# Kernel optimization log

Measured on AMD Instinct MI355X. Metric: run time of the kernel, lower is better.

Reference implementation:

```python
import jax, jax.numpy as jnp
import numpy as np

B, S, D, H = 4, 1024, 1024, 16
HD = D // H


def setup_inputs() -> dict:
    key = jax.random.key(0)
    ks = jax.random.split(key, 8)
    x = jax.random.normal(ks[0], (B, S, D), dtype=jnp.float32)
    attn_bias = jax.random.normal(ks[1], (B, H, S, S), dtype=jnp.float32) * 0.1
    pos_ids = jnp.broadcast_to(jnp.arange(S, dtype=jnp.int32), (B, S))
    lengths = jnp.array([S, S - 64, S - 128, S - 256], dtype=jnp.int32)
    pad_mask = jnp.arange(S)[None, :] >= lengths[:, None]  # True = padded key
    scale = 0.02
    Wq = jax.random.normal(ks[2], (D, D), dtype=jnp.float32) * scale
    Wk = jax.random.normal(ks[3], (D, D), dtype=jnp.float32) * scale
    Wv = jax.random.normal(ks[4], (D, D), dtype=jnp.float32) * scale
    Wo = jax.random.normal(ks[5], (D, D), dtype=jnp.float32) * scale
    bq = jnp.zeros((D,), jnp.float32); bk = jnp.zeros((D,), jnp.float32)
    bv = jnp.zeros((D,), jnp.float32); bo = jnp.zeros((D,), jnp.float32)
    return {"x": x, "attn_bias": attn_bias, "pos_ids": pos_ids, "pad_mask": pad_mask,
            "Wq": Wq, "bq": bq, "Wk": Wk, "bk": bk, "Wv": Wv, "bv": bv, "Wo": Wo, "bo": bo}


def _apply_rotary(q, k, pos_ids):
    # q,k: [B,S,H,HD]; pos_ids: [B,S]
    hd = q.shape[-1]
    inv_freq = 1.0 / (10000.0 ** (jnp.arange(0, hd, 2, dtype=jnp.float32) / hd))
    freqs = pos_ids.astype(jnp.float32)[:, :, None] * inv_freq  # [B,S,HD/2]
    emb = jnp.concatenate([freqs, freqs], axis=-1)[:, :, None, :]  # [B,S,1,HD]
    cos, sin = jnp.cos(emb), jnp.sin(emb)
    def rot_half(t):
        t1, t2 = jnp.split(t, 2, axis=-1)
        return jnp.concatenate([-t2, t1], axis=-1)
    return q * cos + rot_half(q) * sin, k * cos + rot_half(k) * sin


def reference(x, attn_bias, pos_ids, pad_mask, Wq, bq, Wk, bk, Wv, bv, Wo, bo):
    b, s, d = x.shape
    q = (x @ Wq.T + bq).reshape(b, s, H, HD)
    k = (x @ Wk.T + bk).reshape(b, s, H, HD)
    v = (x @ Wv.T + bv).reshape(b, s, H, HD)
    q, k = _apply_rotary(q, k, pos_ids)
    q = q.transpose(0, 2, 1, 3)  # [B,H,S,HD]
    k = k.transpose(0, 2, 1, 3)
    v = v.transpose(0, 2, 1, 3)
    scores = jnp.einsum("bhqd,bhkd->bhqk", q, k) / np.sqrt(HD).astype(np.float32)
    scores = scores + attn_bias
    scores = jnp.where(pad_mask[:, None, None, :], -jnp.inf, scores)
    attn = jax.nn.softmax(scores, axis=-1)  # dropout p=0 -> identity
    out = jnp.einsum("bhqk,bhkd->bqhd", attn, v).reshape(b, s, d)
    metric = k.mean(axis=1)  # mean over heads -> [B,S,HD]
    return out @ Wo.T + bo, metric
```

## Files before the change

kernel.cpp:

```cpp
#include <hip/hip_runtime.h>
#include <hip/hip_bf16.h>

#define SS 1024
#define DD 1024
#define HH 16
#define HDD 64

using f32x4  = __attribute__((ext_vector_type(4))) float;
using bf16x8 = __attribute__((ext_vector_type(8))) __bf16;
using bf16x4 = __attribute__((ext_vector_type(4))) __bf16;

__device__ __forceinline__ void gload_lds16(const void* g, void* l) {
  __builtin_amdgcn_global_load_lds((__attribute__((address_space(1))) void*)g,
                                   (__attribute__((address_space(3))) void*)l, 16, 0, 0);
}

__global__ void convert_kernel(const float4* __restrict__ x, const float4* __restrict__ Wq,
                               const float4* __restrict__ Wk, const float4* __restrict__ Wv,
                               const float4* __restrict__ Wo,
                               bf16x4* __restrict__ xb, bf16x4* __restrict__ wqkvb,
                               bf16x4* __restrict__ wob, float4* __restrict__ metric) {
  int i = blockIdx.x * 256 + threadIdx.x;
  if (blockIdx.x < 256) {
    float4 z = {0.f, 0.f, 0.f, 0.f};
    metric[blockIdx.x * 256 + threadIdx.x] = z;
  }
  float4 v; bf16x4* dst;
  if (i < 1048576)      { v = x[i];              dst = xb + i; }
  else if (i < 1310720) { v = Wq[i - 1048576];   dst = wqkvb + (i - 1048576); }
  else if (i < 1572864) { v = Wk[i - 1310720];   dst = wqkvb + 262144 + (i - 1310720); }
  else if (i < 1835008) { v = Wv[i - 1572864];   dst = wqkvb + 524288 + (i - 1572864); }
  else                  { v = Wo[i - 1835008];   dst = wob + (i - 1835008); }
  bf16x4 o;
  o[0] = (__bf16)v.x; o[1] = (__bf16)v.y; o[2] = (__bf16)v.z; o[3] = (__bf16)v.w;
  *dst = o;
}

template<int EPI, int TN>
__global__ __launch_bounds__(256, 3)
void gemm_kernel(const __bf16* __restrict__ A, const __bf16* __restrict__ Bm, int N,
                 const float* __restrict__ b0, const float* __restrict__ b1,
                 const float* __restrict__ b2, const int* __restrict__ pos_ids,
                 __bf16* __restrict__ Qr, __bf16* __restrict__ Kr, __bf16* __restrict__ Vtg,
                 float* __restrict__ metric, float* __restrict__ Cout) {
  __shared__ __align__(16) char smem[17408];
  __bf16* As = (__bf16*)smem;
  __bf16* Bs = (__bf16*)(smem + 8192);
  constexpr int NJ = TN / 32;
  const int tid = threadIdx.x;
  const int wid = tid >> 6, lane = tid & 63;
  const int g = lane >> 4, cl = lane & 15;
  const int ntn = N / TN;
  const int tile = (blockIdx.x & 7) * ((int)gridDim.x >> 3) + (blockIdx.x >> 3);
  const int bm = tile / ntn, bn = tile % ntn;
  const int m0 = bm << 7, n0 = bn * TN;
  const int wr = (wid >> 1) << 6, wc = (wid & 1) * (TN / 2);

  f32x4 acc[4][NJ] = {};

  for (int kk = 0; kk < 1024; kk += 32) {
    __syncthreads();
#pragma unroll
    for (int p = 0; p < 2; ++p) {
      int idx = p * 256 + tid;
      gload_lds16(A + (size_t)(m0 + (idx >> 2)) * 1024 + kk + ((idx & 3) << 3),
                  (char*)As + p * 4096 + wid * 1024);
    }
#pragma unroll
    for (int p = 0; p < TN / 64; ++p) {
      int idx = p * 256 + tid;
      gload_lds16(Bm + (size_t)(n0 + (idx >> 2)) * 1024 + kk + ((idx & 3) << 3),
                  (char*)Bs + p * 4096 + wid * 1024);
    }
    __syncthreads();
    bf16x8 fa[4], fb[NJ];
#pragma unroll
    for (int i = 0; i < 4; ++i)
      fa[i] = *(const bf16x8*)(As + (wr + i * 16 + cl) * 32 + g * 8);
#pragma unroll
    for (int j = 0; j < NJ; ++j)
      fb[j] = *(const bf16x8*)(Bs + (wc + j * 16 + cl) * 32 + g * 8);
#pragma unroll
    for (int i = 0; i < 4; ++i)
#pragma unroll
      for (int j = 0; j < NJ; ++j)
        acc[i][j] = __builtin_amdgcn_mfma_f32_16x16x32_bf16(fa[i], fb[j], acc[i][j], 0, 0, 0);
  }

  if constexpr (EPI == 1) {
#pragma unroll
    for (int j = 0; j < NJ; ++j) {
      int col = n0 + wc + j * 16 + cl;
      float bv = b0[col];
#pragma unroll
      for (int i = 0; i < 4; ++i)
#pragma unroll
        for (int r = 0; r < 4; ++r) {
          int row = m0 + wr + i * 16 + g * 4 + r;
          Cout[(size_t)row * 1024 + col] = acc[i][j][r] + bv;
        }
    }
  } else if (n0 >= 2048) {
    __bf16* vt_s = (__bf16*)smem;
    const int b_ = m0 >> 10, s0 = m0 & 1023;
    const int vbase = n0 - 2048;
#pragma unroll
    for (int phase = 0; phase < 2; ++phase) {
      __syncthreads();
      if ((wid & 1) == phase) {
#pragma unroll
        for (int j = 0; j < 4; ++j) {
          int d = j * 16 + cl;
          float bv = b2[vbase + wc + d];
#pragma unroll
          for (int i = 0; i < 4; ++i)
#pragma unroll
            for (int r = 0; r < 4; ++r)
              vt_s[d * 136 + wr + i * 16 + g * 4 + r] = (__bf16)(acc[i][j][r] + bv);
        }
      }
      __syncthreads();
      int hh = (vbase >> 6) + phase;
#pragma unroll
      for (int p = 0; p < 4; ++p) {
        int d = p * 16 + (tid >> 4), s8 = (tid & 15) * 8;
        bf16x8 v = *(const bf16x8*)(vt_s + d * 136 + s8);
        *(bf16x8*)(Vtg + ((size_t)(b_ * HH + hh) * HDD + d) * SS + s0 + s8) = v;
      }
    }
  } else {
    const int cb = n0 + wc;
    const int region = cb >> 10;
    const int hcol = (cb & 1023) >> 6;
    const int cir = cb & 1023;
    const float* bias = region == 0 ? b0 : b1;
    __bf16* dst = region == 0 ? Qr : Kr;
    float invf0 = exp2f(-0.4152410118609203f * (float)(cl));
    float invf1 = exp2f(-0.4152410118609203f * (float)(16 + cl));
#pragma unroll
    for (int i = 0; i < 4; ++i) {
#pragma unroll
      for (int r = 0; r < 4; ++r) {
        int row = m0 + wr + i * 16 + g * 4 + r;
        int b_ = row >> 10, s = row & 1023;
        size_t ob = ((size_t)(b_ * HH + hcol) * SS + s) * HDD;
        float pos = (float)pos_ids[row];
#pragma unroll
        for (int j = 0; j < 2; ++j) {
          int dlo = j * 16 + cl;
          float vlo = acc[i][j][r]     + bias[cir + dlo];
          float vhi = acc[i][j + 2][r] + bias[cir + dlo + 32];
          float th = pos * (j == 0 ? invf0 : invf1);
          float sn, cs;
          __sincosf(th, &sn, &cs);
          float olo = vlo * cs - vhi * sn;
          float ohi = vhi * cs + vlo * sn;
          dst[ob + dlo]      = (__bf16)olo;
          dst[ob + dlo + 32] = (__bf16)ohi;
          if (region == 1) {
            atomicAdd(&metric[(size_t)row * HDD + dlo],      olo * 0.0625f);
            atomicAdd(&metric[(size_t)row * HDD + dlo + 32], ohi * 0.0625f);
          }
        }
      }
    }
  }
}

#define TILE_BODY(T, BUF, BCUR, BNXT)                                              \
  {                                                                                \
    __syncthreads();                                                               \
    if ((T) + 1 < ntile) {                                                         \
      const int kk = ((T) + 1) * 64;                                               \
      gload_lds16(Kb + (size_t)(kk + krow) * 64 + kchk * 8,                        \
                  (char*)&Ks[(BUF) ^ 1][8 * wid][0]);                              \
      gload_lds16(Vb + (size_t)krow * SS + kk + kchk * 8,                          \
                  (char*)&Vt[(BUF) ^ 1][8 * wid][0]);                              \
      _Pragma("unroll") for (int kt = 0; kt < 4; ++kt)                             \
        _Pragma("unroll") for (int r = 0; r < 4; ++r)                              \
          BNXT[kt][r] = Bb[(size_t)(q0 + 4 * g + r) * SS + kk + kt * 16 + cl];     \
    }                                                                              \
    f32x4 sc[4];                                                                   \
    __builtin_amdgcn_s_setprio(1);                                                 \
    _Pragma("unroll") for (int kt = 0; kt < 4; ++kt) {                             \
      bf16x8 kb0 = *(const bf16x8*)(&Ks[(BUF)][kt * 16 + cl][(g ^ swz) * 8]);      \
      bf16x8 kb1 = *(const bf16x8*)(&Ks[(BUF)][kt * 16 + cl][((g + 4) ^ swz) * 8]);\
      f32x4 z = {0.f, 0.f, 0.f, 0.f};                                              \
      z = __builtin_amdgcn_mfma_f32_16x16x32_bf16(aq0, kb0, z, 0, 0, 0);           \
      sc[kt] = __builtin_amdgcn_mfma_f32_16x16x32_bf16(aq1, kb1, z, 0, 0, 0);      \
    }                                                                              \
    __builtin_amdgcn_s_setprio(0);                                                 \
    _Pragma("unroll") for (int kt = 0; kt < 4; ++kt)                               \
      _Pragma("unroll") for (int r = 0; r < 4; ++r)                                \
        sc[kt][r] = sc[kt][r] * 0.125f + BCUR[kt][r];                              \
    float mx[4];                                                                   \
    _Pragma("unroll") for (int r = 0; r < 4; ++r)                                  \
      mx[r] = fmaxf(fmaxf(sc[0][r], sc[1][r]), fmaxf(sc[2][r], sc[3][r]));         \
    _Pragma("unroll") for (int d = 1; d < 16; d <<= 1)                             \
      _Pragma("unroll") for (int r = 0; r < 4; ++r)                                \
        mx[r] = fmaxf(mx[r], __shfl_xor(mx[r], d, 64));                            \
    bool adv = true;                                                               \
    _Pragma("unroll") for (int r = 0; r < 4; ++r)                                  \
      adv = adv && (mx[r] <= m_l[r] + 8.0f);                                       \
    if (!__all(adv)) {                                                             \
      _Pragma("unroll") for (int r = 0; r < 4; ++r) {                              \
        float nm = fmaxf(m_l[r], mx[r]);                                           \
        float s_ = __expf(m_l[r] - nm);                                            \
        m_l[r] = nm; l_l[r] *= s_;                                                 \
        _Pragma("unroll") for (int dj = 0; dj < 4; ++dj) o[dj][r] *= s_;           \
      }                                                                            \
    }                                                                              \
    _Pragma("unroll") for (int kt = 0; kt < 4; ++kt)                               \
      _Pragma("unroll") for (int r = 0; r < 4; ++r)                                \
        sc[kt][r] = __expf(sc[kt][r] - m_l[r]);                                    \
    _Pragma("unroll") for (int kt = 0; kt < 4; ++kt)                               \
      _Pragma("unroll") for (int r = 0; r < 4; ++r)                                \
        Plds[wid][g * 4 + r][kt * 16 + cl] = (__bf16)sc[kt][r];                    \
    bf16x8 pa0 = *(const bf16x8*)(&Plds[wid][cl][g * 8]);                          \
    bf16x8 pa1 = *(const bf16x8*)(&Plds[wid][cl][32 + g * 8]);                     \
    __builtin_amdgcn_s_setprio(1);                                                 \
    f32x4 ls = {0.f, 0.f, 0.f, 0.f};                                               \
    ls = __builtin_amdgcn_mfma_f32_16x16x32_bf16(pa0, onesb, ls, 0, 0, 0);         \
    ls = __builtin_amdgcn_mfma_f32_16x16x32_bf16(pa1, onesb, ls, 0, 0, 0);         \
    _Pragma("unroll") for (int dj = 0; dj < 4; ++dj) {                             \
      bf16x8 vb0 = *(const bf16x8*)(&Vt[(BUF)][dj * 16 + cl][(g ^ swz) * 8]);      \
      bf16x8 vb1 = *(const bf16x8*)(&Vt[(BUF)][dj * 16 + cl][((g + 4) ^ swz) * 8]);\
      o[dj] = __builtin_amdgcn_mfma_f32_16x16x32_bf16(pa0, vb0, o[dj], 0, 0, 0);   \
      o[dj] = __builtin_amdgcn_mfma_f32_16x16x32_bf16(pa1, vb1, o[dj], 0, 0, 0);   \
    }                                                                              \
    __builtin_amdgcn_s_setprio(0);                                                 \
    _Pragma("unroll") for (int r = 0; r < 4; ++r) l_l[r] += ls[r];                 \
  }

__global__ __launch_bounds__(512, 4)
void attn_kernel(const __bf16* __restrict__ Qr, const __bf16* __restrict__ Kr,
                 const __bf16* __restrict__ Vtg, const float* __restrict__ bias,
                 const int* __restrict__ pad, __bf16* __restrict__ attn_out) {
  __shared__ __align__(16) __bf16 Ks[2][64][64];
  __shared__ __align__(16) __bf16 Vt[2][64][64];
  __shared__ __align__(16) __bf16 Plds[8][16][68];
  const int tid = threadIdx.x;
  const int wid = tid >> 6, lane = tid & 63;
  const int g = lane >> 4, cl = lane & 15;
  const int bh = blockIdx.x & 63, b_ = bh >> 4, h = bh & 15;
  const int q0 = (blockIdx.x >> 6) * 128 + wid * 16;
  const __bf16* Qb = Qr  + ((size_t)bh << 16);
  const __bf16* Kb = Kr  + ((size_t)bh << 16);
  const __bf16* Vb = Vtg + ((size_t)bh << 16);
  const float*  Bb = bias + ((size_t)bh << 20);
  const int* padb = pad + b_ * SS;

  int pm = (lane < 16) ? padb[lane * 64] : 1;
  unsigned long long ball = __ballot(pm == 0);
  const int ntile = __popcll(ball & 0xFFFFull);

  const int l8 = lane >> 3, l7 = lane & 7;
  const int krow = 8 * wid + l8;
  const int kchk = l7 ^ l8;
  const int swz = cl & 7;

  gload_lds16(Kb + (size_t)krow * 64 + kchk * 8, (char*)&Ks[0][8 * wid][0]);
  gload_lds16(Vb + (size_t)krow * SS + kchk * 8, (char*)&Vt[0][8 * wid][0]);
  float bregA[4][4], bregB[4][4];
#pragma unroll
  for (int kt = 0; kt < 4; ++kt)
#pragma unroll
    for (int r = 0; r < 4; ++r)
      bregA[kt][r] = Bb[(size_t)(q0 + 4 * g + r) * SS + kt * 16 + cl];

  bf16x8 aq0 = *(const bf16x8*)(Qb + (size_t)(q0 + cl) * 64 + g * 8);
  bf16x8 aq1 = *(const bf16x8*)(Qb + (size_t)(q0 + cl) * 64 + 32 + g * 8);
  bf16x8 onesb;
#pragma unroll
  for (int j = 0; j < 8; ++j) onesb[j] = (__bf16)1.0f;

  f32x4 o[4] = {};
  float m_l[4] = {-1e30f, -1e30f, -1e30f, -1e30f};
  float l_l[4] = {0.f, 0.f, 0.f, 0.f};

  for (int t = 0; t < ntile; t += 2) {
    TILE_BODY(t, 0, bregA, bregB);
    if (t + 1 < ntile) TILE_BODY(t + 1, 1, bregB, bregA);
  }

#pragma unroll
  for (int dj = 0; dj < 4; ++dj)
#pragma unroll
    for (int r = 0; r < 4; ++r) {
      int qrow = q0 + g * 4 + r;
      attn_out[(size_t)(b_ * SS + qrow) * DD + h * 64 + dj * 16 + cl] =
          (__bf16)(o[dj][r] / l_l[r]);
    }
}

extern "C" void kernel_launch(void* const* d_in, const int* in_sizes, int n_in,
                              void* d_out, int out_size, void* d_ws, size_t ws_size,
                              hipStream_t stream) {
  const float* x  = (const float*)d_in[0];
  const float* ab = (const float*)d_in[1];
  const int* pos  = (const int*)d_in[2];
  const int* pad  = (const int*)d_in[3];
  const float* Wq = (const float*)d_in[4];
  const float* bq = (const float*)d_in[5];
  const float* Wk = (const float*)d_in[6];
  const float* bk = (const float*)d_in[7];
  const float* Wv = (const float*)d_in[8];
  const float* bv = (const float*)d_in[9];
  const float* Wo = (const float*)d_in[10];
  const float* bo = (const float*)d_in[11];
  float* out = (float*)d_out;
  float* metric = out + 4194304;

  char* ws = (char*)d_ws;
  __bf16* Qr   = (__bf16*)(ws);
  __bf16* Kr   = (__bf16*)(ws + 8388608);
  __bf16* Vtg  = (__bf16*)(ws + 16777216);
  __bf16* xb   = (__bf16*)(ws + 25165824);
  __bf16* wqkv = (__bf16*)(ws + 33554432);
  __bf16* wob  = (__bf16*)(ws + 39845888);
  __bf16* ao   = (__bf16*)(ws + 41943040);

  convert_kernel<<<8192, 256, 0, stream>>>((const float4*)x, (const float4*)Wq,
                                           (const float4*)Wk, (const float4*)Wv,
                                           (const float4*)Wo, (bf16x4*)xb,
                                           (bf16x4*)wqkv, (bf16x4*)wob, (float4*)metric);
  gemm_kernel<0, 128><<<768, 256, 0, stream>>>(xb, wqkv, 3072, bq, bk, bv, pos,
                                               Qr, Kr, Vtg, metric, nullptr);
  attn_kernel<<<512, 512, 0, stream>>>(Qr, Kr, Vtg, ab, pad, ao);
  gemm_kernel<1, 64><<<512, 256, 0, stream>>>(ao, wob, 1024, bo, nullptr, nullptr, nullptr,
                                              nullptr, nullptr, nullptr, nullptr, out);
}
```

Baseline: 173.6 us.

## Double-buffer GEMM LDS tiles with K=64 stages and XOR swizzle

Restructures the bf16 GEMM main loop to use two 32KB LDS buffers with K-step 64, prefetching the next stage via global_load_lds while MFMAs consume the current one, and uses one barrier per iteration. Adds an XOR swizzle on the 16-byte chunk index to reduce LDS bank conflicts on fragment reads. The output projection switches from 128x64 to 128x128 tiles, halving its grid to 256 blocks. The 64KB LDS per block and launch bounds of 2 lower occupancy, and the smaller out-proj grid may underfill the CUs.

Measured after the change: 161.1 us. -7.2%, faster.

```diff
diff --git a/kernel.cpp b/kernel.cpp
--- a/kernel.cpp
+++ b/kernel.cpp
@@ -36,60 +36,69 @@
   *dst = o;
 }
 
-template<int EPI, int TN>
-__global__ __launch_bounds__(256, 3)
+#define GEMM_STAGE(BUF, KK)                                                        \
+  {                                                                                \
+    char* Ab = smem + (BUF) * 32768;                                               \
+    char* Bb = Ab + 16384;                                                         \
+    _Pragma("unroll") for (int q = 0; q < 4; ++q) {                                \
+      int idx = q * 256 + tid;                                                     \
+      int row = idx >> 3, c = idx & 7;                                             \
+      gload_lds16(A  + (size_t)(m0 + row) * 1024 + (KK) + ((c ^ (row & 7)) << 3),  \
+                  Ab + q * 4096 + wid * 1024);                                     \
+      gload_lds16(Bm + (size_t)(n0 + row) * 1024 + (KK) + ((c ^ (row & 7)) << 3),  \
+                  Bb + q * 4096 + wid * 1024);                                     \
+    }                                                                              \
+  }
+
+template<int EPI>
+__global__ __launch_bounds__(256, 2)
 void gemm_kernel(const __bf16* __restrict__ A, const __bf16* __restrict__ Bm, int N,
                  const float* __restrict__ b0, const float* __restrict__ b1,
                  const float* __restrict__ b2, const int* __restrict__ pos_ids,
                  __bf16* __restrict__ Qr, __bf16* __restrict__ Kr, __bf16* __restrict__ Vtg,
                  float* __restrict__ metric, float* __restrict__ Cout) {
-  __shared__ __align__(16) char smem[17408];
-  __bf16* As = (__bf16*)smem;
-  __bf16* Bs = (__bf16*)(smem + 8192);
-  constexpr int NJ = TN / 32;
+  __shared__ __align__(16) char smem[65536];
   const int tid = threadIdx.x;
   const int wid = tid >> 6, lane = tid & 63;
   const int g = lane >> 4, cl = lane & 15;
-  const int ntn = N / TN;
+  const int ntn = N >> 7;
   const int tile = (blockIdx.x & 7) * ((int)gridDim.x >> 3) + (blockIdx.x >> 3);
   const int bm = tile / ntn, bn = tile % ntn;
-  const int m0 = bm << 7, n0 = bn * TN;
-  const int wr = (wid >> 1) << 6, wc = (wid & 1) * (TN / 2);
-
-  f32x4 acc[4][NJ] = {};
-
-  for (int kk = 0; kk < 1024; kk += 32) {
+  const int m0 = bm << 7, n0 = bn << 7;
+  const int wr = (wid >> 1) << 6, wc = (wid & 1) << 6;
+  const int swz = cl & 7;
+
+  f32x4 acc[4][4] = {};
+
+  GEMM_STAGE(0, 0);
+  __syncthreads();
+  int buf = 0;
+  for (int t = 0; t < 16; ++t) {
+    if (t + 1 < 16) GEMM_STAGE(buf ^ 1, (t + 1) * 64);
+    const __bf16* Abuf = (const __bf16*)(smem + buf * 32768);
+    const __bf16* Bbuf = Abuf + 8192;
+#pragma unroll
+    for (int s = 0; s < 2; ++s) {
+      bf16x8 fa[4], fb[4];
+#pragma unroll
+      for (int i = 0; i < 4; ++i)
+        fa[i] = *(const bf16x8*)(Abuf + (wr + i * 16 + cl) * 64 + (((s * 4 + g) ^ swz) << 3));
+#pragma unroll
+      for (int j = 0; j < 4; ++j)
+        fb[j] = *(const bf16x8*)(Bbuf + (wc + j * 16 + cl) * 64 + (((s * 4 + g) ^ swz) << 3));
+#pragma unroll
+      for (int i = 0; i < 4; ++i)
+#pragma unroll
+        for (int j = 0; j < 4; ++j)
+          acc[i][j] = __builtin_amdgcn_mfma_f32_16x16x32_bf16(fa[i], fb[j], acc[i][j], 0, 0, 0);
+    }
     __syncthreads();
-#pragma unroll
-    for (int p = 0; p < 2; ++p) {
-      int idx = p * 256 + tid;
-      gload_lds16(A + (size_t)(m0 + (idx >> 2)) * 1024 + kk + ((idx & 3) << 3),
-                  (char*)As + p * 4096 + wid * 1024);
-    }
-#pragma unroll
-    for (int p = 0; p < TN / 64; ++p) {
-      int idx = p * 256 + tid;
-      gload_lds16(Bm + (size_t)(n0 + (idx >> 2)) * 1024 + kk + ((idx & 3) << 3),
-                  (char*)Bs + p * 4096 + wid * 1024);
-    }
-    __syncthreads();
-    bf16x8 fa[4], fb[NJ];
-#pragma unroll
-    for (int i = 0; i < 4; ++i)
-      fa[i] = *(const bf16x8*)(As + (wr + i * 16 + cl) * 32 + g * 8);
-#pragma unroll
-    for (int j = 0; j < NJ; ++j)
-      fb[j] = *(const bf16x8*)(Bs + (wc + j * 16 + cl) * 32 + g * 8);
-#pragma unroll
-    for (int i = 0; i < 4; ++i)
-#pragma unroll
-      for (int j = 0; j < NJ; ++j)
-        acc[i][j] = __builtin_amdgcn_mfma_f32_16x16x32_bf16(fa[i], fb[j], acc[i][j], 0, 0, 0);
+    buf ^= 1;
   }
 
   if constexpr (EPI == 1) {
 #pragma unroll
-    for (int j = 0; j < NJ; ++j) {
+    for (int j = 0; j < 4; ++j) {
       int col = n0 + wc + j * 16 + cl;
       float bv = b0[col];
 #pragma unroll
@@ -324,9 +333,9 @@
                                            (const float4*)Wk, (const float4*)Wv,
                                            (const float4*)Wo, (bf16x4*)xb,
                                            (bf16x4*)wqkv, (bf16x4*)wob, (float4*)metric);
-  gemm_kernel<0, 128><<<768, 256, 0, stream>>>(xb, wqkv, 3072, bq, bk, bv, pos,
-                                               Qr, Kr, Vtg, metric, nullptr);
+  gemm_kernel<0><<<768, 256, 0, stream>>>(xb, wqkv, 3072, bq, bk, bv, pos,
+                                          Qr, Kr, Vtg, metric, nullptr);
   attn_kernel<<<512, 512, 0, stream>>>(Qr, Kr, Vtg, ab, pad, ao);
-  gemm_kernel<1, 64><<<512, 256, 0, stream>>>(ao, wob, 1024, bo, nullptr, nullptr, nullptr,
-                                              nullptr, nullptr, nullptr, nullptr, out);
-}
+  gemm_kernel<1><<<256, 256, 0, stream>>>(ao, wob, 1024, bo, nullptr, nullptr, nullptr,
+                                          nullptr, nullptr, nullptr, nullptr, out);
+}
```
